# Kernel tuning notes

Measured on AMD Instinct MI355X. Metric: run time of the kernel, lower is better.

The kernel has to match this reference:

```python
import jax, jax.numpy as jnp
import numpy as np

N, E, B = 4096, 4096, 128  # nodes, edges, graphs


def _param(key, shape, scale):
    return jax.random.normal(key, shape, dtype=jnp.float32) * scale


def setup_inputs() -> dict:
    key = jax.random.key(0)
    ks = jax.random.split(key, 32)
    inp = {
        "x": jax.random.normal(ks[0], (N, 37), dtype=jnp.float32),
        "edge_index": jax.random.randint(ks[1], (2, E), 0, N),
        "edge_attr": jax.random.uniform(ks[2], (E, 5), dtype=jnp.float32),
        "batch": jnp.sort(jax.random.randint(ks[3], (N,), 0, B)),
        # NNConv 1: edge-MLP 5->512->37*128, root [37,128]
        "nn1_w1": _param(ks[4], (5, 512), 0.3),
        "nn1_b1": jnp.zeros((512,), jnp.float32),
        "nn1_w2": _param(ks[5], (512, 37 * 128), 0.01),
        "nn1_b2": jnp.zeros((37 * 128,), jnp.float32),
        "root1": _param(ks[6], (37, 128), 0.1),
        "bias1": jnp.zeros((128,), jnp.float32),
        # NNConv 2: edge-MLP 5->128->128*256, root [128,256]
        "nn2_w1": _param(ks[7], (5, 128), 0.3),
        "nn2_b1": jnp.zeros((128,), jnp.float32),
        "nn2_w2": _param(ks[8], (128, 128 * 256), 0.005),
        "nn2_b2": jnp.zeros((128 * 256,), jnp.float32),
        "root2": _param(ks[9], (128, 256), 0.05),
        "bias2": jnp.zeros((256,), jnp.float32),
        # NNConv 3: edge-MLP 5->128->256*256, root [256,256]
        "nn3_w1": _param(ks[10], (5, 128), 0.3),
        "nn3_b1": jnp.zeros((128,), jnp.float32),
        "nn3_w2": _param(ks[11], (128, 256 * 256), 0.005),
        "nn3_b2": jnp.zeros((256 * 256,), jnp.float32),
        "root3": _param(ks[12], (256, 256), 0.05),
        "bias3": jnp.zeros((256,), jnp.float32),
        # readout MLP
        "fc1_w": _param(ks[13], (256, 128), 0.06),
        "fc1_b": jnp.zeros((128,), jnp.float32),
        "fc2_w": _param(ks[14], (128, 64), 0.09),
        "fc2_b": jnp.zeros((64,), jnp.float32),
        "fc3_w": _param(ks[15], (64, 1), 0.12),
        "fc3_b": jnp.zeros((1,), jnp.float32),
    }
    return inp


def _nnconv(x, src, dst, edge_attr, w1, b1, w2, b2, root, bias, cin, cout):
    # edge MLP -> per-edge weight matrix [E, cin, cout]
    h = jax.nn.relu(edge_attr @ w1 + b1)
    W = (h @ w2 + b2).reshape(-1, cin, cout)
    # gather source features, per-edge matvec, scatter-add to targets
    msg = jnp.einsum('ei,eio->eo', x[src], W)          # [E, cout]
    agg = jax.ops.segment_sum(msg, dst, num_segments=x.shape[0])
    return agg + x @ root + bias


def _segment_mean(x, seg, num_segments):
    s = jax.ops.segment_sum(x, seg, num_segments=num_segments)
    cnt = jax.ops.segment_sum(jnp.ones((x.shape[0],), x.dtype), seg,
                              num_segments=num_segments)
    return s / jnp.maximum(cnt, 1.0)[:, None]


def reference(x, edge_index, edge_attr, batch,
              nn1_w1, nn1_b1, nn1_w2, nn1_b2, root1, bias1,
              nn2_w1, nn2_b1, nn2_w2, nn2_b2, root2, bias2,
              nn3_w1, nn3_b1, nn3_w2, nn3_b2, root3, bias3,
              fc1_w, fc1_b, fc2_w, fc2_b, fc3_w, fc3_b):
    src, dst = edge_index[0], edge_index[1]
    h = jax.nn.elu(_nnconv(x, src, dst, edge_attr, nn1_w1, nn1_b1, nn1_w2,
                           nn1_b2, root1, bias1, 37, 128))
    h = jax.nn.elu(_nnconv(h, src, dst, edge_attr, nn2_w1, nn2_b1, nn2_w2,
                           nn2_b2, root2, bias2, 128, 256))
    h = jax.nn.elu(_nnconv(h, src, dst, edge_attr, nn3_w1, nn3_b1, nn3_w2,
                           nn3_b2, root3, bias3, 256, 256))
    g = _segment_mean(h, batch, B)                     # [B, 256]
    g = jax.nn.elu(g @ fc1_w + fc1_b)
    g = jax.nn.elu(g @ fc2_w + fc2_b)
    g = g @ fc3_w + fc3_b
    return g.reshape(-1)
```

## Files before the change

### kernel.cpp

```cpp
#include <hip/hip_runtime.h>
#include <cstdint>
#include <cstddef>

typedef float f32x4 __attribute__((ext_vector_type(4)));
typedef _Float16 f16x8 __attribute__((ext_vector_type(8)));
typedef _Float16 f16x4 __attribute__((ext_vector_type(4)));

__device__ __forceinline__ float elu_f(float x) { return x > 0.f ? x : expm1f(x); }

__device__ __forceinline__ void gload_lds16(const void* g, void* l)
{
    __builtin_amdgcn_global_load_lds(
        (const __attribute__((address_space(1))) void*)g,
        (__attribute__((address_space(3))) void*)l,
        16, 0, 0);
}

template <int CIN, int COUT, int KFTOT>
__device__ __forceinline__
void pack_body(int bid, int tid, const float* __restrict__ w2, const float* __restrict__ b2,
               _Float16* __restrict__ w2h, int KH, float* tile )
{
    const int kh = bid / KFTOT;
    const int c  = bid - kh * KFTOT;
    const int CP = 32 * COUT;
    for (int i = tid; i < CP; i += 256) {
        int kk = i / COUT, n = i - kk * COUT;
        int kg = c * 32 + kk;
        float v = 0.f;
        if (kg < CIN) v = (kh < KH) ? w2[((size_t)kh * CIN + kg) * COUT + n]
                                    : b2[(size_t)kg * COUT + n];
        tile[kk * (COUT + 2) + n] = v;
    }
    __syncthreads();
    _Float16* outp = w2h + (size_t)bid * CP;
    for (int i = tid; i < CP; i += 256) {
        int n = i >> 5, kk = i & 31;
        int blk = (kk >> 3) ^ ((n >> 1) & 3);
        outp[n * 32 + blk * 8 + (kk & 7)] = (_Float16)tile[kk * (COUT + 2) + n];
    }
}

__global__ __launch_bounds__(256)
void uber_prologue_kernel(const float* __restrict__ ea,
                          const int* __restrict__ dst, int* __restrict__ cnt,
                          const float* __restrict__ w1a, const float* __restrict__ b1a, _Float16* __restrict__ h1T,
                          const float* __restrict__ w1b, const float* __restrict__ b1b, _Float16* __restrict__ h2T,
                          const float* __restrict__ w1c, const float* __restrict__ b1c, _Float16* __restrict__ h3T,
                          int E,
                          const float* __restrict__ w2a, const float* __restrict__ b2a, _Float16* __restrict__ w2h1,
                          const float* __restrict__ w2b, const float* __restrict__ b2b, _Float16* __restrict__ w2h2,
                          const float* __restrict__ w2c, const float* __restrict__ b2c, _Float16* __restrict__ w2h3)
{
    __shared__ __align__(16) float smem[32 * 258];
    const int tid = threadIdx.x;
    const int nEB = E >> 6;
    int b = blockIdx.x;

    if (b < nEB) {
        const int e0 = b * 64;
        const int el = tid & 63;
        const int cg = tid >> 6;
        if (tid < 64) atomicAdd(&cnt[dst[e0 + tid]], 1);
        float* a = smem;
        for (int i = tid; i < 320; i += 256) a[(i / 5) * 5 + (i % 5)] = ea[e0 * 5 + i];
        __syncthreads();
        float av[5];
        #pragma unroll
        for (int j = 0; j < 5; ++j) av[j] = a[el * 5 + j];
        #pragma unroll 4
        for (int t = 0; t < 128; ++t) {
            const int ch = t * 4 + cg;
            float s = b1a[ch];
            #pragma unroll
            for (int j = 0; j < 5; ++j) s = fmaf(av[j], w1a[j * 512 + ch], s);
            h1T[(size_t)ch * E + e0 + el] = (_Float16)fmaxf(s, 0.f);
        }
        #pragma unroll 4
        for (int t = 0; t < 32; ++t) {
            const int ch = t * 4 + cg;
            float s = b1b[ch];
            float u = b1c[ch];
            #pragma unroll
            for (int j = 0; j < 5; ++j) {
                s = fmaf(av[j], w1b[j * 128 + ch], s);
                u = fmaf(av[j], w1c[j * 128 + ch], u);
            }
            h2T[(size_t)ch * E + e0 + el] = (_Float16)fmaxf(s, 0.f);
            h3T[(size_t)ch * E + e0 + el] = (_Float16)fmaxf(u, 0.f);
        }
        return;
    }
    b -= nEB;
    if (b < 513 * 2) { pack_body<37, 128, 2>(b, tid, w2a, b2a, w2h1, 512, smem); return; }
    b -= 513 * 2;
    if (b < 129 * 4) { pack_body<128, 256, 4>(b, tid, w2b, b2b, w2h2, 128, smem); return; }
    b -= 129 * 4;
    pack_body<256, 256, 8>(b, tid, w2c, b2c, w2h3, 128, smem);
}

__global__ __launch_bounds__(256)
void csr_scan_graph_kernel(const int* __restrict__ cnt, int* __restrict__ offs, int N,
                           const int* __restrict__ batch, int* __restrict__ goffs, int B,
                           int NN)
{
    __shared__ int sums[256];
    __shared__ int pref[257];
    const int tid = threadIdx.x;
    const int per = N / 256;
    int loc = 0;
    for (int i = 0; i < per; ++i) loc += cnt[tid * per + i];
    sums[tid] = loc;
    __syncthreads();
    if (tid == 0) {
        int s = 0; pref[0] = 0;
        for (int i = 0; i < 256; ++i) { s += sums[i]; pref[i + 1] = s; }
    }
    __syncthreads();
    int run = pref[tid];
    for (int i = 0; i < per; ++i) { offs[tid * per + i] = run; run += cnt[tid * per + i]; }
    if (tid == 255) offs[N] = run;
    for (int g = tid; g <= B; g += 256) {
        int lo = 0, hi = NN;
        while (lo < hi) { int mid = (lo + hi) >> 1; if (batch[mid] < g) lo = mid + 1; else hi = mid; }
        goffs[g] = lo;
    }
}

__global__ __launch_bounds__(256)
void csr_fill_kernel(const int* __restrict__ dst, const int* __restrict__ offs,
                     int* __restrict__ cur, int* __restrict__ eid, int E)
{
    int e = blockIdx.x * 256 + threadIdx.x;
    if (e < E) {
        int d = dst[e];
        int p = offs[d] + atomicAdd(&cur[d], 1);
        eid[p] = e;
    }
}

template <int KH, int CIN, int COUT, int KFTOT, int CSPLIT, int NY>
__global__ __launch_bounds__(256, 4)
void msg_mfma_kernel(const float* __restrict__ xin,
                     const _Float16* __restrict__ hT,
                     const _Float16* __restrict__ w2h,
                     const int* __restrict__ src,
                     _Float16* __restrict__ part,
                     int E, int khg_per)
{
    constexpr int BM = 256;
    constexpr int KF = KFTOT / CSPLIT;

    __shared__ __align__(16) _Float16 bsh[2][KF][64][32];
    __shared__ _Float16 s_h[2][BM];
    __shared__ int s_src[BM];

    const int tid  = threadIdx.x;
    const int lane = tid & 63;
    const int w    = tid >> 6;
    const int l15  = lane & 15;
    const int lg   = lane >> 4;
    const int swb  = (l15 >> 1) & 3;

    const int nwg = gridDim.x;
    const int bid = blockIdx.x;
    const int swz = (bid & 7) * (nwg >> 3) + (bid >> 3);
    const int m    = swz & 15;
    const int rest = swz >> 4;
    const int y    = rest % NY;
    const int zz   = rest / NY;
    const int cinH = zz % CSPLIT;
    const int zkh  = zz / CSPLIT;

    const int e0  = m * BM;
    const int n0  = y * 64;
    const int k0  = cinH * KF * 32;
    const int kh0 = zkh * khg_per;
    const int kh1 = min(kh0 + khg_per, KH + 1);

    s_src[tid] = src[e0 + tid];
    __syncthreads();

    f16x8 a_[4][KF];
    #pragma unroll
    for (int mf = 0; mf < 4; ++mf) {
        const int eloc = w * 64 + mf * 16 + l15;
        const float* xrow = xin + (size_t)s_src[eloc] * CIN + k0;
        #pragma unroll
        for (int c = 0; c < KF; ++c) {
            if (CIN % 32 == 0) {
                float4 p0 = *(const float4*)(xrow + c * 32 + lg * 8);
                float4 p1 = *(const float4*)(xrow + c * 32 + lg * 8 + 4);
                a_[mf][c][0] = (_Float16)p0.x; a_[mf][c][1] = (_Float16)p0.y;
                a_[mf][c][2] = (_Float16)p0.z; a_[mf][c][3] = (_Float16)p0.w;
                a_[mf][c][4] = (_Float16)p1.x; a_[mf][c][5] = (_Float16)p1.y;
                a_[mf][c][6] = (_Float16)p1.z; a_[mf][c][7] = (_Float16)p1.w;
            } else {
                #pragma unroll
                for (int j = 0; j < 8; ++j) {
                    int kk = c * 32 + lg * 8 + j;
                    float v = (k0 + kk < CIN) ? xrow[kk] : 0.f;
                    a_[mf][c][j] = (_Float16)v;
                }
            }
        }
    }

    f32x4 msg[4][4];
    #pragma unroll
    for (int mf = 0; mf < 4; ++mf)
        #pragma unroll
        for (int nf = 0; nf < 4; ++nf) msg[mf][nf] = 0.f;

    auto stage = [&](int khg, int pp) {
        if (khg >= kh1) return;
        const size_t chunk0 = (size_t)khg * KFTOT + cinH * KF;
        const char* g = (const char*)(w2h + (chunk0 * COUT + n0) * 32) + (size_t)tid * 16;
        char* l = (char*)(&bsh[pp][0][0][0]) + (tid >> 6) * 1024;
        #pragma unroll
        for (int c = 0; c < KF; ++c)
            gload_lds16(g + (size_t)c * COUT * 64, l + c * 4096);
    };
    auto stage_h = [&](int khg) {
        if (khg < kh1 && khg < KH) s_h[khg & 1][tid] = hT[(size_t)khg * E + e0 + tid];
    };

    int p = 0;
    stage(kh0, 0);
    stage_h(kh0);

    for (int khg = kh0; khg < kh1; ++khg) {
        __syncthreads();

        stage(khg + 1, p ^ 1);
        stage_h(khg + 1);

        _Float16 hh[4];
        #pragma unroll
        for (int mf = 0; mf < 4; ++mf)
            hh[mf] = (khg < KH) ? s_h[khg & 1][w * 64 + mf * 16 + l15] : (_Float16)1.0f;

        #pragma unroll
        for (int c = 0; c < KF; ++c) {
            f16x8 Bv[4];
            #pragma unroll
            for (int nf = 0; nf < 4; ++nf)
                Bv[nf] = *(const f16x8*)&bsh[p][c][nf * 16 + l15][(lg ^ swb) * 8];
            #pragma unroll
            for (int mf = 0; mf < 4; ++mf) {
                f16x8 ah = a_[mf][c] * hh[mf];
                #pragma unroll
                for (int nf = 0; nf < 4; ++nf)
                    msg[mf][nf] = __builtin_amdgcn_mfma_f32_16x16x32_f16(ah, Bv[nf], msg[mf][nf], 0, 0, 0);
            }
        }
        p ^= 1;
    }

    _Float16* pb = part + ((size_t)zz * E + e0) * COUT + n0;
    #pragma unroll
    for (int mf = 0; mf < 4; ++mf)
        #pragma unroll
        for (int r = 0; r < 4; ++r) {
            const int row = w * 64 + mf * 16 + lg * 4 + r;
            #pragma unroll
            for (int nf = 0; nf < 4; ++nf)
                pb[(size_t)row * COUT + nf * 16 + l15] = (_Float16)msg[mf][nf][r];
        }
}

template <int CIN, int COUT, int Z>
__global__ __launch_bounds__(256)
void node_gemm_kernel(const float* __restrict__ xin,
                      const float* __restrict__ root,
                      const _Float16* __restrict__ part,
                      const int* __restrict__ offs,
                      const int* __restrict__ eid,
                      const float* __restrict__ bias,
                      float* __restrict__ out, int E)
{
    constexpr int BM  = 64;
    constexpr int BN  = 64;
    constexpr int BKI = (CIN % 32 == 0) ? 32 : 16;
    constexpr int CIN_PAD = ((CIN + BKI - 1) / BKI) * BKI;
    constexpr int CPK = CIN_PAD / BKI;
    constexpr int NROWS = BKI / 16;

    __shared__ __align__(16) float xs_t[CIN_PAD][BM];
    __shared__ __align__(16) float btile[BKI][BN];

    const int tid = threadIdx.x;
    const int tx  = tid & 15;
    const int ty  = tid >> 4;
    const int ty4 = ty * 4;
    const int tx4 = tx * 4;
    const int e0  = blockIdx.x * BM;
    const int n0  = blockIdx.y * BN;

    for (int idx = tid; idx < BM * CIN_PAD; idx += 256) {
        int mm = idx / CIN_PAD;
        int i  = idx - mm * CIN_PAD;
        float v = 0.f;
        if (i < CIN) v = xin[(size_t)(e0 + mm) * CIN + i];
        xs_t[i][mm] = v;
    }

    const int rbase = tid >> 4;
    const int nn    = (tid & 15) * 4;
    float acc[4][4] = {};
    float4 pre[NROWS];

    {
        const float* brow = root + n0;
        #pragma unroll
        for (int rr = 0; rr < NROWS; ++rr) {
            int r = rbase + rr * 16;
            float4 v = {0.f, 0.f, 0.f, 0.f};
            if (r < CIN) v = *(const float4*)(brow + (size_t)r * COUT + nn);
            pre[rr] = v;
        }
    }

    for (int c = 0; c < CPK; ++c) {
        __syncthreads();
        #pragma unroll
        for (int rr = 0; rr < NROWS; ++rr)
            *(float4*)&btile[rbase + rr * 16][nn] = pre[rr];
        __syncthreads();

        if (c + 1 < CPK) {
            int i0n = (c + 1) * BKI;
            const float* brow = root + (size_t)i0n * COUT + n0;
            #pragma unroll
            for (int rr = 0; rr < NROWS; ++rr) {
                int r = rbase + rr * 16;
                float4 v = {0.f, 0.f, 0.f, 0.f};
                if (i0n + r < CIN) v = *(const float4*)(brow + (size_t)r * COUT + nn);
                pre[rr] = v;
            }
        }

        const int i0 = c * BKI;
        #pragma unroll
        for (int ii = 0; ii < BKI; ++ii) {
            float4 xv = *(const float4*)&xs_t[i0 + ii][ty4];
            float4 bv = *(const float4*)&btile[ii][tx4];
            float av[4] = {xv.x, xv.y, xv.z, xv.w};
            float bvv[4] = {bv.x, bv.y, bv.z, bv.w};
            #pragma unroll
            for (int mm = 0; mm < 4; ++mm)
                #pragma unroll
                for (int nq = 0; nq < 4; ++nq)
                    acc[mm][nq] = fmaf(av[mm], bvv[nq], acc[mm][nq]);
        }
    }

    float bs[4];
    #pragma unroll
    for (int nq = 0; nq < 4; ++nq) bs[nq] = bias[n0 + tx4 + nq];

    #pragma unroll
    for (int mm = 0; mm < 4; ++mm) {
        const int row = e0 + ty4 + mm;
        float add[4] = {0.f, 0.f, 0.f, 0.f};
        const int b = offs[row], t = offs[row + 1];
        for (int j = b; j < t; ++j) {
            const int e = eid[j];
            #pragma unroll
            for (int z = 0; z < Z; ++z) {
                f16x4 r4 = *(const f16x4*)(part + ((size_t)z * E + e) * COUT + n0 + tx4);
                add[0] += (float)r4.x; add[1] += (float)r4.y;
                add[2] += (float)r4.z; add[3] += (float)r4.w;
            }
        }
        size_t base = (size_t)row * COUT + n0 + tx4;
        #pragma unroll
        for (int nq = 0; nq < 4; ++nq)
            out[base + nq] = elu_f(acc[mm][nq] + add[nq] + bs[nq]);
    }
}

__global__ __launch_bounds__(256)
void pool_readout_kernel(const float* __restrict__ hl3, const int* __restrict__ goffs,
                         const float* __restrict__ fc1w, const float* __restrict__ fc1b,
                         const float* __restrict__ fc2w, const float* __restrict__ fc2b,
                         const float* __restrict__ fc3w, const float* __restrict__ fc3b,
                         float* __restrict__ outp)
{
    const int g   = blockIdx.x;
    const int tid = threadIdx.x;
    __shared__ float gm[256];
    __shared__ float a1[128];
    __shared__ float a2[64];
    const int b = goffs[g], t = goffs[g + 1];
    float s = 0.f;
    for (int n = b; n < t; ++n) s += hl3[(size_t)n * 256 + tid];
    gm[tid] = s / fmaxf((float)(t - b), 1.f);
    __syncthreads();
    if (tid < 128) {
        float v = fc1b[tid];
        for (int j = 0; j < 256; ++j) v = fmaf(gm[j], fc1w[j * 128 + tid], v);
        a1[tid] = elu_f(v);
    }
    __syncthreads();
    if (tid < 64) {
        float v = fc2b[tid];
        for (int j = 0; j < 128; ++j) v = fmaf(a1[j], fc2w[j * 64 + tid], v);
        a2[tid] = elu_f(v);
    }
    __syncthreads();
    if (tid == 0) {
        float v = fc3b[0];
        for (int j = 0; j < 64; ++j) v = fmaf(a2[j], fc3w[j], v);
        outp[g] = v;
    }
}

extern "C" void kernel_launch(void* const* d_in, const int* in_sizes, int n_in,
                              void* d_out, int out_size, void* d_ws, size_t ws_size,
                              hipStream_t stream)
{
    const float* x      = (const float*)d_in[0];
    const int*   ei     = (const int*)  d_in[1];
    const float* ea     = (const float*)d_in[2];
    const int*   batch  = (const int*)  d_in[3];
    const float* nn1_w1 = (const float*)d_in[4];
    const float* nn1_b1 = (const float*)d_in[5];
    const float* nn1_w2 = (const float*)d_in[6];
    const float* nn1_b2 = (const float*)d_in[7];
    const float* root1  = (const float*)d_in[8];
    const float* bias1  = (const float*)d_in[9];
    const float* nn2_w1 = (const float*)d_in[10];
    const float* nn2_b1 = (const float*)d_in[11];
    const float* nn2_w2 = (const float*)d_in[12];
    const float* nn2_b2 = (const float*)d_in[13];
    const float* root2  = (const float*)d_in[14];
    const float* bias2  = (const float*)d_in[15];
    const float* nn3_w1 = (const float*)d_in[16];
    const float* nn3_b1 = (const float*)d_in[17];
    const float* nn3_w2 = (const float*)d_in[18];
    const float* nn3_b2 = (const float*)d_in[19];
    const float* root3  = (const float*)d_in[20];
    const float* bias3  = (const float*)d_in[21];
    const float* fc1_w  = (const float*)d_in[22];
    const float* fc1_b  = (const float*)d_in[23];
    const float* fc2_w  = (const float*)d_in[24];
    const float* fc2_b  = (const float*)d_in[25];
    const float* fc3_w  = (const float*)d_in[26];
    const float* fc3_b  = (const float*)d_in[27];

    const int E = in_sizes[2] / 5;
    const int N = in_sizes[0] / 37;
    const int B = out_size;
    const int* srcp = ei;
    const int* dstp = ei + E;

    const size_t W1H = (size_t)513 * 2 * 128 * 32;
    const size_t W2H = (size_t)129 * 4 * 256 * 32;
    const size_t W3H = (size_t)129 * 8 * 256 * 32;
    _Float16* w2h1 = (_Float16*)d_ws;
    _Float16* w2h2 = w2h1 + W1H;
    _Float16* w2h3 = w2h2 + W2H;
    _Float16* h1T  = w2h3 + W3H;
    _Float16* h2T  = h1T + (size_t)512 * E;
    _Float16* h3T  = h2T + (size_t)128 * E;
    _Float16* part = h3T + (size_t)128 * E;
    float* fbase = (float*)(part + (size_t)32 * E * 128);
    float* hl1   = fbase;
    float* hl2   = hl1 + (size_t)N * 128;
    float* hl3   = hl2 + (size_t)N * 256;
    int* ibase   = (int*)(hl3 + (size_t)N * 256);
    int* cnt   = ibase;
    int* cur   = cnt + N;
    int* offs  = cur + N;
    int* eid   = offs + N + 1;
    int* goffs = eid + E;

    hipMemsetAsync(cnt, 0, 2 * N * sizeof(int), stream);

    const int nEB = E / 64;
    uber_prologue_kernel<<<nEB + 1026 + 516 + 1032, 256, 0, stream>>>(
        ea, dstp, cnt,
        nn1_w1, nn1_b1, h1T, nn2_w1, nn2_b1, h2T, nn3_w1, nn3_b1, h3T, E,
        nn1_w2, nn1_b2, w2h1, nn2_w2, nn2_b2, w2h2, nn3_w2, nn3_b2, w2h3);

    csr_scan_graph_kernel<<<1, 256, 0, stream>>>(cnt, offs, N, batch, goffs, B, N);
    csr_fill_kernel<<<(E + 255) / 256, 256, 0, stream>>>(dstp, offs, cur, eid, E);

    msg_mfma_kernel<512, 37, 128, 2, 1, 2><<<1024, 256, 0, stream>>>(
        x, h1T, w2h1, srcp, part, E, 17);
    node_gemm_kernel<37, 128, 32><<<dim3(N / 64, 2), 256, 0, stream>>>(
        x, root1, part, offs, eid, bias1, hl1, E);

    msg_mfma_kernel<128, 128, 256, 4, 2, 4><<<1024, 256, 0, stream>>>(
        hl1, h2T, w2h2, srcp, part, E, 17);
    node_gemm_kernel<128, 256, 16><<<dim3(N / 64, 4), 256, 0, stream>>>(
        hl1, root2, part, offs, eid, bias2, hl2, E);

    msg_mfma_kernel<128, 256, 256, 8, 4, 4><<<1024, 256, 0, stream>>>(
        hl2, h3T, w2h3, srcp, part, E, 33);
    node_gemm_kernel<256, 256, 16><<<dim3(N / 64, 4), 256, 0, stream>>>(
        hl2, root3, part, offs, eid, bias3, hl3, E);

    pool_readout_kernel<<<B, 256, 0, stream>>>(hl3, goffs, fc1_w, fc1_b,
                                               fc2_w, fc2_b, fc3_w, fc3_b,
                                               (float*)d_out);
}
```

Measured before the change: 292.1 us.

## Triple-buffer msg MFMA weight staging and halve node GEMM row tile

```diff
diff --git a/kernel.cpp b/kernel.cpp
--- a/kernel.cpp
+++ b/kernel.cpp
@@ -151,8 +151,7 @@
     constexpr int BM = 256;
     constexpr int KF = KFTOT / CSPLIT;
 
-    __shared__ __align__(16) _Float16 bsh[2][KF][64][32];
-    __shared__ _Float16 s_h[2][BM];
+    __shared__ __align__(16) _Float16 bsh[3][KF][64][32];
     __shared__ int s_src[BM];
 
     const int tid  = threadIdx.x;
@@ -221,31 +220,36 @@
         for (int c = 0; c < KF; ++c)
             gload_lds16(g + (size_t)c * COUT * 64, l + c * 4096);
     };
-    auto stage_h = [&](int khg) {
-        if (khg < kh1 && khg < KH) s_h[khg & 1][tid] = hT[(size_t)khg * E + e0 + tid];
-    };
-
-    int p = 0;
+
     stage(kh0, 0);
-    stage_h(kh0);
-
+    stage(kh0 + 1, 1);
+
+    int bi = 0;
     for (int khg = kh0; khg < kh1; ++khg) {
-        __syncthreads();
-
-        stage(khg + 1, p ^ 1);
-        stage_h(khg + 1);
+        asm volatile("s_waitcnt vmcnt(2)" ::: "memory");
+        __builtin_amdgcn_s_barrier();
 
         _Float16 hh[4];
-        #pragma unroll
-        for (int mf = 0; mf < 4; ++mf)
-            hh[mf] = (khg < KH) ? s_h[khg & 1][w * 64 + mf * 16 + l15] : (_Float16)1.0f;
-
+        if (khg < KH) {
+            const _Float16* hp = hT + (size_t)khg * E + e0 + w * 64 + l15;
+            #pragma unroll
+            for (int mf = 0; mf < 4; ++mf) hh[mf] = hp[mf * 16];
+        } else {
+            #pragma unroll
+            for (int mf = 0; mf < 4; ++mf) hh[mf] = (_Float16)1.0f;
+        }
+        __builtin_amdgcn_sched_barrier(0);
+
+        int bi2 = bi + 2; if (bi2 >= 3) bi2 -= 3;
+        stage(khg + 2, bi2);
+
+        __builtin_amdgcn_s_setprio(1);
         #pragma unroll
         for (int c = 0; c < KF; ++c) {
             f16x8 Bv[4];
             #pragma unroll
             for (int nf = 0; nf < 4; ++nf)
-                Bv[nf] = *(const f16x8*)&bsh[p][c][nf * 16 + l15][(lg ^ swb) * 8];
+                Bv[nf] = *(const f16x8*)&bsh[bi][c][nf * 16 + l15][(lg ^ swb) * 8];
             #pragma unroll
             for (int mf = 0; mf < 4; ++mf) {
                 f16x8 ah = a_[mf][c] * hh[mf];
@@ -254,7 +258,9 @@
                     msg[mf][nf] = __builtin_amdgcn_mfma_f32_16x16x32_f16(ah, Bv[nf], msg[mf][nf], 0, 0, 0);
             }
         }
-        p ^= 1;
+        __builtin_amdgcn_s_setprio(0);
+
+        ++bi; if (bi == 3) bi = 0;
     }
 
     _Float16* pb = part + ((size_t)zz * E + e0) * COUT + n0;
@@ -279,7 +285,7 @@
                       const float* __restrict__ bias,
                       float* __restrict__ out, int E)
 {
-    constexpr int BM  = 64;
+    constexpr int BM  = 32;
     constexpr int BN  = 64;
     constexpr int BKI = (CIN % 32 == 0) ? 32 : 16;
     constexpr int CIN_PAD = ((CIN + BKI - 1) / BKI) * BKI;
@@ -292,7 +298,7 @@
     const int tid = threadIdx.x;
     const int tx  = tid & 15;
     const int ty  = tid >> 4;
-    const int ty4 = ty * 4;
+    const int ty2 = ty * 2;
     const int tx4 = tx * 4;
     const int e0  = blockIdx.x * BM;
     const int n0  = blockIdx.y * BN;
@@ -307,7 +313,7 @@
 
     const int rbase = tid >> 4;
     const int nn    = (tid & 15) * 4;
-    float acc[4][4] = {};
+    float acc[2][4] = {};
     float4 pre[NROWS];
 
     {
@@ -343,12 +349,12 @@
         const int i0 = c * BKI;
         #pragma unroll
         for (int ii = 0; ii < BKI; ++ii) {
-            float4 xv = *(const float4*)&xs_t[i0 + ii][ty4];
+            float2 xv = *(const float2*)&xs_t[i0 + ii][ty2];
             float4 bv = *(const float4*)&btile[ii][tx4];
-            float av[4] = {xv.x, xv.y, xv.z, xv.w};
+            float av[2] = {xv.x, xv.y};
             float bvv[4] = {bv.x, bv.y, bv.z, bv.w};
             #pragma unroll
-            for (int mm = 0; mm < 4; ++mm)
+            for (int mm = 0; mm < 2; ++mm)
                 #pragma unroll
                 for (int nq = 0; nq < 4; ++nq)
                     acc[mm][nq] = fmaf(av[mm], bvv[nq], acc[mm][nq]);
@@ -360,8 +366,8 @@
     for (int nq = 0; nq < 4; ++nq) bs[nq] = bias[n0 + tx4 + nq];
 
     #pragma unroll
-    for (int mm = 0; mm < 4; ++mm) {
-        const int row = e0 + ty4 + mm;
+    for (int mm = 0; mm < 2; ++mm) {
+        const int row = e0 + ty2 + mm;
         float add[4] = {0.f, 0.f, 0.f, 0.f};
         const int b = offs[row], t = offs[row + 1];
         for (int j = b; j < t; ++j) {
@@ -489,17 +495,17 @@
 
     msg_mfma_kernel<512, 37, 128, 2, 1, 2><<<1024, 256, 0, stream>>>(
         x, h1T, w2h1, srcp, part, E, 17);
-    node_gemm_kernel<37, 128, 32><<<dim3(N / 64, 2), 256, 0, stream>>>(
+    node_gemm_kernel<37, 128, 32><<<dim3(N / 32, 2), 256, 0, stream>>>(
         x, root1, part, offs, eid, bias1, hl1, E);
 
     msg_mfma_kernel<128, 128, 256, 4, 2, 4><<<1024, 256, 0, stream>>>(
         hl1, h2T, w2h2, srcp, part, E, 17);
-    node_gemm_kernel<128, 256, 16><<<dim3(N / 64, 4), 256, 0, stream>>>(
+    node_gemm_kernel<128, 256, 16><<<dim3(N / 32, 4), 256, 0, stream>>>(
         hl1, root2, part, offs, eid, bias2, hl2, E);
 
     msg_mfma_kernel<128, 256, 256, 8, 4, 4><<<1024, 256, 0, stream>>>(
         hl2, h3T, w2h3, srcp, part, E, 33);
-    node_gemm_kernel<256, 256, 16><<<dim3(N / 64, 4), 256, 0, stream>>>(
+    node_gemm_kernel<256, 256, 16><<<dim3(N / 32, 4), 256, 0, stream>>>(
         hl2, root3, part, offs, eid, bias3, hl3, E);
 
     pool_readout_kernel<<<B, 256, 0, stream>>>(hl3, goffs, fc1_w, fc1_b,
```

Result: slower. 304.4 us (+4.2%).

## Load edge-MLP weight tiles directly from global memory instead of LDS double-buffering

Applied to the files above, without the earlier changes.

```diff
diff --git a/kernel.cpp b/kernel.cpp
--- a/kernel.cpp
+++ b/kernel.cpp
@@ -7,14 +7,6 @@
 typedef _Float16 f16x4 __attribute__((ext_vector_type(4)));
 
 __device__ __forceinline__ float elu_f(float x) { return x > 0.f ? x : expm1f(x); }
-
-__device__ __forceinline__ void gload_lds16(const void* g, void* l)
-{
-    __builtin_amdgcn_global_load_lds(
-        (const __attribute__((address_space(1))) void*)g,
-        (__attribute__((address_space(3))) void*)l,
-        16, 0, 0);
-}
 
 template <int CIN, int COUT, int KFTOT>
 __device__ __forceinline__
@@ -36,8 +28,7 @@
     _Float16* outp = w2h + (size_t)bid * CP;
     for (int i = tid; i < CP; i += 256) {
         int n = i >> 5, kk = i & 31;
-        int blk = (kk >> 3) ^ ((n >> 1) & 3);
-        outp[n * 32 + blk * 8 + (kk & 7)] = (_Float16)tile[kk * (COUT + 2) + n];
+        outp[n * 32 + kk] = (_Float16)tile[kk * (COUT + 2) + n];
     }
 }
 
@@ -150,9 +141,8 @@
 {
     constexpr int BM = 256;
     constexpr int KF = KFTOT / CSPLIT;
-
-    __shared__ __align__(16) _Float16 bsh[2][KF][64][32];
-    __shared__ _Float16 s_h[2][BM];
+    static_assert(KF == 1, "direct-L2 msg kernel expects one 32-k chunk per block");
+
     __shared__ int s_src[BM];
 
     const int tid  = threadIdx.x;
@@ -160,7 +150,6 @@
     const int w    = tid >> 6;
     const int l15  = lane & 15;
     const int lg   = lane >> 4;
-    const int swb  = (l15 >> 1) & 3;
 
     const int nwg = gridDim.x;
     const int bid = blockIdx.x;
@@ -174,34 +163,31 @@
 
     const int e0  = m * BM;
     const int n0  = y * 64;
-    const int k0  = cinH * KF * 32;
+    const int k0  = cinH * 32;
     const int kh0 = zkh * khg_per;
     const int kh1 = min(kh0 + khg_per, KH + 1);
 
     s_src[tid] = src[e0 + tid];
     __syncthreads();
 
-    f16x8 a_[4][KF];
+    f16x8 a_[4];
     #pragma unroll
     for (int mf = 0; mf < 4; ++mf) {
         const int eloc = w * 64 + mf * 16 + l15;
         const float* xrow = xin + (size_t)s_src[eloc] * CIN + k0;
-        #pragma unroll
-        for (int c = 0; c < KF; ++c) {
-            if (CIN % 32 == 0) {
-                float4 p0 = *(const float4*)(xrow + c * 32 + lg * 8);
-                float4 p1 = *(const float4*)(xrow + c * 32 + lg * 8 + 4);
-                a_[mf][c][0] = (_Float16)p0.x; a_[mf][c][1] = (_Float16)p0.y;
-                a_[mf][c][2] = (_Float16)p0.z; a_[mf][c][3] = (_Float16)p0.w;
-                a_[mf][c][4] = (_Float16)p1.x; a_[mf][c][5] = (_Float16)p1.y;
-                a_[mf][c][6] = (_Float16)p1.z; a_[mf][c][7] = (_Float16)p1.w;
-            } else {
-                #pragma unroll
-                for (int j = 0; j < 8; ++j) {
-                    int kk = c * 32 + lg * 8 + j;
-                    float v = (k0 + kk < CIN) ? xrow[kk] : 0.f;
-                    a_[mf][c][j] = (_Float16)v;
-                }
+        if (CIN % 32 == 0) {
+            float4 p0 = *(const float4*)(xrow + lg * 8);
+            float4 p1 = *(const float4*)(xrow + lg * 8 + 4);
+            a_[mf][0] = (_Float16)p0.x; a_[mf][1] = (_Float16)p0.y;
+            a_[mf][2] = (_Float16)p0.z; a_[mf][3] = (_Float16)p0.w;
+            a_[mf][4] = (_Float16)p1.x; a_[mf][5] = (_Float16)p1.y;
+            a_[mf][6] = (_Float16)p1.z; a_[mf][7] = (_Float16)p1.w;
+        } else {
+            #pragma unroll
+            for (int j = 0; j < 8; ++j) {
+                int kk = lg * 8 + j;
+                float v = (k0 + kk < CIN) ? xrow[kk] : 0.f;
+                a_[mf][j] = (_Float16)v;
             }
         }
     }
@@ -212,49 +198,33 @@
         #pragma unroll
         for (int nf = 0; nf < 4; ++nf) msg[mf][nf] = 0.f;
 
-    auto stage = [&](int khg, int pp) {
-        if (khg >= kh1) return;
-        const size_t chunk0 = (size_t)khg * KFTOT + cinH * KF;
-        const char* g = (const char*)(w2h + (chunk0 * COUT + n0) * 32) + (size_t)tid * 16;
-        char* l = (char*)(&bsh[pp][0][0][0]) + (tid >> 6) * 1024;
-        #pragma unroll
-        for (int c = 0; c < KF; ++c)
-            gload_lds16(g + (size_t)c * COUT * 64, l + c * 4096);
-    };
-    auto stage_h = [&](int khg) {
-        if (khg < kh1 && khg < KH) s_h[khg & 1][tid] = hT[(size_t)khg * E + e0 + tid];
-    };
-
-    int p = 0;
-    stage(kh0, 0);
-    stage_h(kh0);
+    const int bro = l15 * 32 + lg * 8;
 
     for (int khg = kh0; khg < kh1; ++khg) {
-        __syncthreads();
-
-        stage(khg + 1, p ^ 1);
-        stage_h(khg + 1);
+        const _Float16* cb = w2h + ((size_t)(khg * KFTOT + cinH) * COUT + n0) * 32;
+
+        f16x8 Bv[4];
+        #pragma unroll
+        for (int nf = 0; nf < 4; ++nf)
+            Bv[nf] = *(const f16x8*)(cb + nf * 512 + bro);
 
         _Float16 hh[4];
-        #pragma unroll
-        for (int mf = 0; mf < 4; ++mf)
-            hh[mf] = (khg < KH) ? s_h[khg & 1][w * 64 + mf * 16 + l15] : (_Float16)1.0f;
-
-        #pragma unroll
-        for (int c = 0; c < KF; ++c) {
-            f16x8 Bv[4];
+        if (khg < KH) {
+            const _Float16* hp = hT + (size_t)khg * E + e0 + w * 64 + l15;
+            #pragma unroll
+            for (int mf = 0; mf < 4; ++mf) hh[mf] = hp[mf * 16];
+        } else {
+            #pragma unroll
+            for (int mf = 0; mf < 4; ++mf) hh[mf] = (_Float16)1.0f;
+        }
+
+        #pragma unroll
+        for (int mf = 0; mf < 4; ++mf) {
+            f16x8 ah = a_[mf] * hh[mf];
             #pragma unroll
             for (int nf = 0; nf < 4; ++nf)
-                Bv[nf] = *(const f16x8*)&bsh[p][c][nf * 16 + l15][(lg ^ swb) * 8];
-            #pragma unroll
-            for (int mf = 0; mf < 4; ++mf) {
-                f16x8 ah = a_[mf][c] * hh[mf];
-                #pragma unroll
-                for (int nf = 0; nf < 4; ++nf)
-                    msg[mf][nf] = __builtin_amdgcn_mfma_f32_16x16x32_f16(ah, Bv[nf], msg[mf][nf], 0, 0, 0);
-            }
-        }
-        p ^= 1;
+                msg[mf][nf] = __builtin_amdgcn_mfma_f32_16x16x32_f16(ah, Bv[nf], msg[mf][nf], 0, 0, 0);
+        }
     }
 
     _Float16* pb = part + ((size_t)zz * E + e0) * COUT + n0;
@@ -487,18 +457,18 @@
     csr_scan_graph_kernel<<<1, 256, 0, stream>>>(cnt, offs, N, batch, goffs, B, N);
     csr_fill_kernel<<<(E + 255) / 256, 256, 0, stream>>>(dstp, offs, cur, eid, E);
 
-    msg_mfma_kernel<512, 37, 128, 2, 1, 2><<<1024, 256, 0, stream>>>(
-        x, h1T, w2h1, srcp, part, E, 17);
+    msg_mfma_kernel<512, 37, 128, 2, 2, 2><<<1024, 256, 0, stream>>>(
+        x, h1T, w2h1, srcp, part, E, 33);
     node_gemm_kernel<37, 128, 32><<<dim3(N / 64, 2), 256, 0, stream>>>(
         x, root1, part, offs, eid, bias1, hl1, E);
 
-    msg_mfma_kernel<128, 128, 256, 4, 2, 4><<<1024, 256, 0, stream>>>(
-        hl1, h2T, w2h2, srcp, part, E, 17);
+    msg_mfma_kernel<128, 128, 256, 4, 4, 4><<<1024, 256, 0, stream>>>(
+        hl1, h2T, w2h2, srcp, part, E, 33);
     node_gemm_kernel<128, 256, 16><<<dim3(N / 64, 4), 256, 0, stream>>>(
         hl1, root2, part, offs, eid, bias2, hl2, E);
 
-    msg_mfma_kernel<128, 256, 256, 8, 4, 4><<<1024, 256, 0, stream>>>(
-        hl2, h3T, w2h3, srcp, part, E, 33);
+    msg_mfma_kernel<128, 256, 256, 8, 8, 4><<<1024, 256, 0, stream>>>(
+        hl2, h3T, w2h3, srcp, part, E, 65);
     node_gemm_kernel<256, 256, 16><<<dim3(N / 64, 4), 256, 0, stream>>>(
         hl2, root3, part, offs, eid, bias3, hl3, E);
 
```

Result: slower. 324.5 us (+11.1%).
